# Performance work log

Measured on AMD Instinct MI355X. Metric: run time of the kernel, lower is better.

## Reference

```python
import jax, jax.numpy as jnp
import numpy as np
from jax import lax

B, CIN, HID, COUT = 64, 256, 256, 10
MULTI, KS = 3, 3
TH = TW = 7      # template (kernel) input spatial size
SH = SW = 31     # search input spatial size
EPS = 1e-5
DN = ('NCHW', 'OIHW', 'NCHW')


def _conv(x, w):
    return lax.conv_general_dilated(x, w, (1, 1), 'VALID', dimension_numbers=DN)


def _bn(x, p):
    # p: [4, C] packed (gamma, beta, running_mean, running_var); inference-mode BN
    g, b, m, v = p[0], p[1], p[2], p[3]
    inv = g / jnp.sqrt(v + EPS)
    return x * inv[:, None, None] + (b - m * inv)[:, None, None]


def _dwxcorr(x, k):
    # per-sample depthwise cross-correlation via groups = B*C trick
    b, c, h, w = x.shape
    kh, kw = k.shape[2], k.shape[3]
    y = lax.conv_general_dilated(
        x.reshape(1, b * c, h, w), k.reshape(b * c, 1, kh, kw),
        (1, 1), 'VALID', dimension_numbers=DN, feature_group_count=b * c)
    return y.reshape(b, c, y.shape[2], y.shape[3])


def _multixcorr(search, kernel):
    # crop template feature to 5x5 / 3x3 / 1x1 sub-kernels, xcorr each,
    # center-crop outputs to the common (smallest) size, concat on channels
    kh = kernel.shape[2]
    feats = []
    for i in range(MULTI):
        kk = kernel[:, :, i:kh - i, i:kh - i]
        o = _dwxcorr(search, kk)
        if i > 0:
            o = o[:, :, i:o.shape[2] - i, i:o.shape[3] - i]
        feats.append(o)
    return jnp.concatenate(feats, axis=1)  # [B, MULTI*HID, 25, 25]


def setup_inputs() -> dict:
    key = jax.random.key(0)
    ks = jax.random.split(key, 12)
    f32 = jnp.float32
    return {
        'kernel': jax.random.normal(ks[0], (B, CIN, TH, TW), f32),
        'search': jax.random.normal(ks[1], (B, CIN, SH, SW), f32),
        'wk': jax.random.normal(ks[2], (HID, CIN, KS, KS), f32) * 0.05,
        'bnk': jax.random.uniform(ks[3], (4, HID), f32, 0.1, 1.0),
        'ws': jax.random.normal(ks[4], (HID, CIN, KS, KS), f32) * 0.05,
        'bns': jax.random.uniform(ks[5], (4, HID), f32, 0.1, 1.0),
        'wd': jax.random.normal(ks[6], (HID, CIN * MULTI, 1, 1), f32) * 0.05,
        'bnd': jax.random.uniform(ks[7], (4, HID), f32, 0.1, 1.0),
        'wh1': jax.random.normal(ks[8], (HID, HID, 1, 1), f32) * 0.05,
        'bnh': jax.random.uniform(ks[9], (4, HID), f32, 0.1, 1.0),
        'wh2': jax.random.normal(ks[10], (COUT, HID, 1, 1), f32) * 0.05,
        'bh2': jax.random.normal(ks[11], (COUT,), f32) * 0.05,
    }


def reference(kernel, search, wk, bnk, ws, bns, wd, bnd, wh1, bnh, wh2, bh2):
    k = jax.nn.relu(_bn(_conv(kernel, wk), bnk))   # [B, HID, 5, 5]
    s = jax.nn.relu(_bn(_conv(search, ws), bns))   # [B, HID, 29, 29]
    feature = _multixcorr(s, k)                    # [B, 3*HID, 25, 25]
    feature = _bn(_conv(feature, wd), bnd)         # [B, HID, 25, 25]
    h = jax.nn.relu(_bn(_conv(feature, wh1), bnh))
    out = _conv(h, wh2) + bh2[:, None, None]       # [B, COUT, 25, 25]
    return out
```

## Files before the change

kernel.cpp:

```cpp
#include <hip/hip_runtime.h>
#include <hip/hip_bf16.h>
#include <cstdint>
#include <cstddef>

#define EPSBN 1e-5f

typedef unsigned short u16;
typedef unsigned int u32;
typedef _Float16 f16;
typedef _Float16 f16x8 __attribute__((ext_vector_type(8)));
typedef float f32x4 __attribute__((ext_vector_type(4)));

__device__ __forceinline__ void async_copy16(void* lds, const void* g) {
    __builtin_amdgcn_global_load_lds(
        (const __attribute__((address_space(1))) u32*)g,
        (__attribute__((address_space(3))) u32*)lds, 16, 0, 0);
}

__global__ __launch_bounds__(256) void prep_all(
    const float* __restrict__ sin, f16* __restrict__ sa,
    const float* __restrict__ kin, f16* __restrict__ ka,
    const float* __restrict__ wk, const float* __restrict__ ws,
    const float* __restrict__ wd, const float* __restrict__ wh1,
    const float* __restrict__ wh2, f16* __restrict__ bpk,
    f16* __restrict__ bps, f16* __restrict__ bpd, f16* __restrict__ bp1,
    f16* __restrict__ bp2) {
    __shared__ float tile[64][65];
    int t = blockIdx.x;
    int tid = threadIdx.x;
    if (t < 4352) {
        int b = t / 68;
        int rem = t - b * 68;
        int c0 = (rem / 17) * 64;
        int z = rem % 17;
        bool isk = (z == 16);
        const float* in = isk ? kin : sin;
        f16* op = isk ? ka : sa;
        int HW = isk ? 49 : 961;
        int h0 = isk ? 0 : z * 64;
        int cl = tid >> 6;
        int hl = tid & 63;
        for (int r = cl; r < 64; r += 4) {
            int hw = h0 + hl;
            tile[r][hl] =
                (hw < HW) ? in[(size_t)(b * 256 + c0 + r) * HW + hw] : 0.f;
        }
        __syncthreads();
        int c = tid & 63;
        for (int r = cl; r < 64; r += 4) {
            int hw = h0 + r;
            if (hw < HW)
                op[((size_t)b * HW + hw) * 256 + c0 + c] = (f16)tile[c][r];
        }
        return;
    }
    int blk = t - 4352;
    const float* W;
    f16* Bp;
    int nK32, OCr, K, i;
    bool conv = false;
    if (blk < 2304) {
        W = wk; Bp = bpk; nK32 = 72; OCr = 256; K = 2304; conv = true;
        i = blk * 256 + tid;
    } else if (blk < 4608) {
        W = ws; Bp = bps; nK32 = 72; OCr = 256; K = 2304; conv = true;
        i = (blk - 2304) * 256 + tid;
    } else if (blk < 5376) {
        W = wd; Bp = bpd; nK32 = 24; OCr = 256; K = 768;
        i = (blk - 4608) * 256 + tid;
    } else if (blk < 5632) {
        W = wh1; Bp = bp1; nK32 = 8; OCr = 256; K = 256;
        i = (blk - 5376) * 256 + tid;
    } else {
        W = wh2; Bp = bp2; nK32 = 8; OCr = 10; K = 256;
        i = (blk - 5632) * 256 + tid;
    }
    int per = nK32 * 512;
    int oct = i / per;
    int r = i - oct * per;
    int k32 = r >> 9;
    int lr = r & 511;
    int l = lr >> 3, j = lr & 7;
    int oc = oct * 16 + (l & 15);
    int k = k32 * 32 + ((l >> 4) << 3) + j;
    float v = 0.f;
    if (oc < OCr)
        v = conv ? W[(size_t)(oc * 256 + (k & 255)) * 9 + (k >> 8)]
                 : W[(size_t)oc * K + k];
    Bp[(size_t)(oct * nK32 + k32) * 512 + lr] = (f16)v;
}

template <int KHW, int EPI>
__device__ __forceinline__ void gemm8_body(
    f16* lds, const f16* __restrict__ A, const f16* __restrict__ Bp,
    const float* __restrict__ bnp, float* __restrict__ outF,
    f16* __restrict__ oF, int m0, int M, int OC, int C, int H, int W,
    int OH, int OW) {
    const int Ktot = KHW * C;
    const int nKt = Ktot >> 6;
    const int nI = nKt >> 1;
    const int nK32 = Ktot >> 5;
    const int tid = threadIdx.x;
    const int lane = tid & 63;
    const int wid = tid >> 6;
    const int rowl = lane & 15;
    const int quad = lane >> 4;
    const int wm = wid >> 2;
    const int wn = wid & 3;
    const int OHW = OH * OW;

    int arow[4];
#pragma unroll
    for (int h = 0; h < 2; ++h)
#pragma unroll
        for (int s = 0; s < 2; ++s) {
            int ml = ((wid & 4) << 5) + h * 64 + (wid & 3) * 16 + s * 8 +
                     (lane >> 3);
            int m = m0 + ml;
            if (m >= M) m = M - 1;
            int b = m / OHW;
            int r = m - b * OHW;
            int y = r / OW;
            int x = r - y * OW;
            arow[h * 2 + s] = ((b * H + y) * W + x) * C +
                              (((lane & 7) ^ (lane >> 3)) << 3);
        }
    int bsrcb[2];
#pragma unroll
    for (int h = 0; h < 2; ++h) {
        int slot = h * 8 + wid;
        int o = ((slot >> 1) & 3) * 4 + ((slot >> 3) << 1) + (slot & 1);
        bsrcb[h] = o * nK32 * 512 + lane * 8;
    }

    auto koff_of = [&](int kt) {
        if (KHW == 9) {
            int pos = kt >> 2;
            int ky = pos / 3, kx = pos - ky * 3;
            return (ky * W + kx) * C + ((kt & 3) << 6);
        }
        return kt << 6;
    };
    auto stageA = [&](int buf, int h, int kt) {
        int koff = koff_of(kt);
#pragma unroll
        for (int s = 0; s < 2; ++s)
            async_copy16(
                &lds[buf * 16384 +
                     ((h * 1024 + wid * 128 + s * 64 + lane) << 3)],
                A + arow[h * 2 + s] + koff);
    };
    auto stageB = [&](int buf, int h, int kt) {
#pragma unroll
        for (int s = 0; s < 2; ++s)
            async_copy16(
                &lds[32768 + buf * 16384 +
                     ((((h * 8 + wid) * 2 + s) * 64 + lane) << 3)],
                Bp + bsrcb[h] + (kt * 2 + s) * 512);
    };

    f32x4 acc[8][4];
#pragma unroll
    for (int i = 0; i < 8; ++i)
#pragma unroll
        for (int j = 0; j < 4; ++j) acc[i][j] = (f32x4)0.f;

    f16x8 ah[4][2], bhA[2][2], bhB[2][2];

    auto dsA = [&](int buf, int qm) {
#pragma unroll
        for (int ii = 0; ii < 4; ++ii) {
            int g = qm * 128 + wm * 64 + ii * 16 + rowl;
#pragma unroll
            for (int ks = 0; ks < 2; ++ks)
                ah[ii][ks] = *(const f16x8*)&lds[
                    buf * 16384 + g * 64 +
                    ((((ks << 2) | quad) ^ (rowl & 7)) << 3)];
        }
    };
    auto dsB = [&](int buf, int qn, f16x8 (&bh)[2][2]) {
#pragma unroll
        for (int jj = 0; jj < 2; ++jj) {
            int slot = qn * 8 + wn * 2 + jj;
#pragma unroll
            for (int ks = 0; ks < 2; ++ks)
                bh[jj][ks] = *(const f16x8*)&lds[
                    32768 + buf * 16384 + (slot * 2 + ks) * 512 + lane * 8];
        }
    };

#define MFMA_QUAD(qm, qn, bh)                                            \
    do {                                                                 \
        _Pragma("unroll") for (int ks = 0; ks < 2; ++ks)                 \
            _Pragma("unroll") for (int ii = 0; ii < 4; ++ii)             \
                _Pragma("unroll") for (int jj = 0; jj < 2; ++jj)         \
                    acc[(qm)*4 + ii][(qn)*2 + jj] =                      \
                        __builtin_amdgcn_mfma_f32_16x16x32_f16(          \
                            ah[ii][ks], bh[jj][ks],                      \
                            acc[(qm)*4 + ii][(qn)*2 + jj], 0, 0, 0);     \
    } while (0)

#define PH_TAIL(MF)                                        \
    __builtin_amdgcn_s_barrier();                          \
    asm volatile("s_waitcnt lgkmcnt(0)" ::: "memory");     \
    __builtin_amdgcn_s_setprio(1);                         \
    MF;                                                    \
    __builtin_amdgcn_s_setprio(0)

    stageA(0, 0, 0);
    stageA(0, 1, 0);
    stageB(0, 0, 0);
    stageB(0, 1, 0);
    stageA(1, 0, 1);
    stageB(1, 0, 1);
    stageB(1, 1, 1);
    asm volatile("s_waitcnt vmcnt(6)" ::: "memory");
    __builtin_amdgcn_s_barrier();

    for (int it = 0; it < nI; ++it) {
        const bool more = (it + 1 < nI);
        const int t2 = 2 * it + 2;
        const int t3 = 2 * it + 3;
        dsA(0, 0);
        dsB(0, 0, bhA);
        stageA(1, 1, 2 * it + 1);
        PH_TAIL(MFMA_QUAD(0, 0, bhA));
        __builtin_amdgcn_s_barrier();
        dsB(0, 1, bhB);
        if (more) stageA(0, 0, t2);
        PH_TAIL(MFMA_QUAD(0, 1, bhB));
        __builtin_amdgcn_s_barrier();
        dsA(0, 1);
        if (more) stageB(0, 0, t2);
        PH_TAIL(MFMA_QUAD(1, 0, bhA));
        __builtin_amdgcn_s_barrier();
        if (more) stageB(0, 1, t2);
        PH_TAIL(MFMA_QUAD(1, 1, bhB));
        if (more)
            asm volatile("s_waitcnt vmcnt(6)" ::: "memory");
        else
            asm volatile("s_waitcnt vmcnt(0)" ::: "memory");
        __builtin_amdgcn_s_barrier();
        dsA(1, 0);
        dsB(1, 0, bhA);
        if (more) stageA(0, 1, t2);
        PH_TAIL(MFMA_QUAD(0, 0, bhA));
        __builtin_amdgcn_s_barrier();
        dsB(1, 1, bhB);
        if (more) stageA(1, 0, t3);
        PH_TAIL(MFMA_QUAD(0, 1, bhB));
        __builtin_amdgcn_s_barrier();
        dsA(1, 1);
        if (more) stageB(1, 0, t3);
        PH_TAIL(MFMA_QUAD(1, 0, bhA));
        __builtin_amdgcn_s_barrier();
        if (more) stageB(1, 1, t3);
        PH_TAIL(MFMA_QUAD(1, 1, bhB));
        if (more) asm volatile("s_waitcnt vmcnt(6)" ::: "memory");
        __builtin_amdgcn_s_barrier();
    }
#undef PH_TAIL
#undef MFMA_QUAD

#pragma unroll
    for (int j = 0; j < 4; ++j) {
        int oc = wn * 64 + j * 16 + rowl;
        bool ocv = oc < OC;
        float scale = 1.f, shift = 0.f;
        if (ocv) {
            if (EPI != 3) {
                float g = bnp[oc];
                float bb = bnp[OC + oc];
                float mm = bnp[2 * OC + oc];
                float vv = bnp[3 * OC + oc];
                float inv = g * rsqrtf(vv + EPSBN);
                scale = inv;
                shift = bb - mm * inv;
            } else {
                shift = bnp[oc];
            }
        }
#pragma unroll
        for (int i = 0; i < 8; ++i) {
#pragma unroll
            for (int r = 0; r < 4; ++r) {
                int m = m0 + wm * 128 + i * 16 + quad * 4 + r;
                if (m < M && ocv) {
                    float v = acc[i][j][r] * scale + shift;
                    if (EPI == 2) v = fmaxf(v, 0.f);
                    if (EPI == 3) {
                        int b = m / OHW;
                        int rr = m - b * OHW;
                        outF[((size_t)b * OC + oc) * OHW + rr] = v;
                    } else {
                        oF[(size_t)m * OC + oc] = (f16)v;
                    }
                }
            }
        }
    }
}

__global__ __launch_bounds__(512, 2) void conv33_fused8(
    const f16* sA_g, const f16* bpS, const float* bns, f16* sOut,
    const f16* kA_g, const f16* bpK, const float* bnk, f16* kOut) {
    __shared__ f16 lds[65536];
    bool sec = blockIdx.x < 7;
    const f16* A = sec ? kA_g : sA_g;
    const f16* Bp = sec ? bpK : bpS;
    const float* bnp = sec ? bnk : bns;
    f16* oF = sec ? kOut : sOut;
    int M = sec ? 1600 : 53824;
    int Hh = sec ? 7 : 31;
    int OHs = sec ? 5 : 29;
    int m0 = (sec ? blockIdx.x : (blockIdx.x - 7)) * 256;
    gemm8_body<9, 2>(lds, A, Bp, bnp, nullptr, oF, m0, M, 256, 256, Hh, Hh,
                     OHs, OHs);
}

template <int KHW, int EPI>
__device__ __forceinline__ void gemm_body(
    f16* sA, const f16* __restrict__ A, const f16* __restrict__ Bp,
    const float* __restrict__ bnp, float* __restrict__ outF,
    f16* __restrict__ oF, int m0, int n0, int M, int OC, int C, int H, int W,
    int OH, int OW) {
    const int Ktot = KHW * C;
    const int nKb = Ktot >> 7;
    const int nK32 = Ktot >> 5;
    const int tid = threadIdx.x;
    const int OHW = OH * OW;

    int abase[8];
#pragma unroll
    for (int s = 0; s < 8; ++s) {
        int idx = tid + s * 256;
        int ml = idx >> 4;
        int qs = (idx & 15) ^ (ml & 15);
        int m = m0 + ml;
        if (m >= M) m = M - 1;
        int b = m / OHW;
        int r = m - b * OHW;
        int y = r / OW;
        int x = r - y * OW;
        abase[s] = ((b * H + y) * W + x) * C + qs * 8;
    }

    f32x4 acc[4][4];
#pragma unroll
    for (int i = 0; i < 4; ++i)
#pragma unroll
        for (int j = 0; j < 4; ++j) acc[i][j] = (f32x4)0.f;

    const int lane = tid & 63;
    const int row = lane & 15;
    const int quad = lane >> 4;
    const int wv = tid >> 6;
    const int wm = (wv & 1) * 64;
    const int wn = (wv >> 1) * 64;
    const int octb = (n0 + wn) >> 4;

    auto koff_of = [&](int kb) {
        if (KHW == 9) {
            int pos = kb >> 1;
            int cin0 = (kb & 1) << 7;
            int ky = pos / 3;
            int kx = pos - ky * 3;
            return (ky * W + kx) * C + cin0;
        }
        return kb << 7;
    };
    auto issueA = [&](int bufbase, int kb) {
        int koff = koff_of(kb);
#pragma unroll
        for (int s = 0; s < 8; ++s)
            async_copy16(&sA[bufbase + tid * 8 + s * 2048],
                         A + abase[s] + koff);
    };
    auto loadB = [&](f16x8(&bh)[4][4], int kb) {
#pragma unroll
        for (int ks = 0; ks < 4; ++ks)
#pragma unroll
            for (int j = 0; j < 4; ++j)
                bh[ks][j] =
                    *(const f16x8*)&Bp[((size_t)(octb + j) * nK32 + kb * 4 +
                                        ks) *
                                           512 +
                                       lane * 8];
    };
    auto compute = [&](int bufbase, f16x8(&bh)[4][4]) {
#pragma unroll
        for (int ks = 0; ks < 4; ++ks) {
            f16x8 ah[4];
#pragma unroll
            for (int i = 0; i < 4; ++i) {
                int g = wm + i * 16 + row;
                ah[i] = *(const f16x8*)&sA[bufbase + g * 128 +
                                           ((((ks << 2) | quad) ^ row) << 3)];
            }
#pragma unroll
            for (int i = 0; i < 4; ++i)
#pragma unroll
                for (int j = 0; j < 4; ++j)
                    acc[i][j] = __builtin_amdgcn_mfma_f32_16x16x32_f16(
                        ah[i], bh[ks][j], acc[i][j], 0, 0, 0);
        }
    };

    f16x8 bh0[4][4], bh1[4][4];
    issueA(0, 0);
    loadB(bh0, 0);
    for (int kb = 0; kb < nKb; kb += 2) {
        __syncthreads();
        issueA(16384, kb + 1);
        loadB(bh1, kb + 1);
        compute(0, bh0);
        __syncthreads();
        if (kb + 2 < nKb) {
            issueA(0, kb + 2);
            loadB(bh0, kb + 2);
        }
        compute(16384, bh1);
    }

#pragma unroll
    for (int j = 0; j < 4; ++j) {
        int oc = n0 + wn + j * 16 + row;
        bool ocv = oc < OC;
        float scale = 1.f, shift = 0.f;
        if (ocv) {
            if (EPI != 3) {
                float g = bnp[oc];
                float bb = bnp[OC + oc];
                float mm = bnp[2 * OC + oc];
                float vv = bnp[3 * OC + oc];
                float inv = g * rsqrtf(vv + EPSBN);
                scale = inv;
                shift = bb - mm * inv;
            } else {
                shift = bnp[oc];
            }
        }
#pragma unroll
        for (int i = 0; i < 4; ++i) {
#pragma unroll
            for (int r = 0; r < 4; ++r) {
                int m = m0 + wm + i * 16 + quad * 4 + r;
                if (m < M && ocv) {
                    float v = acc[i][j][r] * scale + shift;
                    if (EPI == 2) v = fmaxf(v, 0.f);
                    if (EPI == 3) {
                        int b = m / OHW;
                        int rr = m - b * OHW;
                        outF[((size_t)b * OC + oc) * OHW + rr] = v;
                    } else {
                        oF[(size_t)m * OC + oc] = (f16)v;
                    }
                }
            }
        }
    }
}

template <int EPI>
__global__ __launch_bounds__(256, 2) void gemm_1x1(
    const f16* __restrict__ A, const f16* __restrict__ Bp,
    const float* __restrict__ bnp, float* __restrict__ outF,
    f16* __restrict__ oF, int M, int OC, int C) {
    __shared__ f16 sA[32768];
    gemm_body<1, EPI>(sA, A, Bp, bnp, outF, oF, blockIdx.x * 128,
                      blockIdx.y * 128, M, OC, C, 25, 25, 25, 25);
}

__global__ __launch_bounds__(256) void xcorr_nhwc(
    const f16* __restrict__ sf, const f16* __restrict__ kf,
    f16* __restrict__ feat) {
    int by = blockIdx.x;
    int b = by / 25;
    int y = by - b * 25;
    int c = threadIdx.x;
    float kv[25];
#pragma unroll
    for (int p = 0; p < 25; ++p)
        kv[p] = (float)kf[(size_t)(b * 25 + p) * 256 + c];
    const f16* srow = sf + (size_t)(b * 29 + y) * 29 * 256 + c;
    float sv[25];
#pragma unroll
    for (int d = 0; d < 5; ++d)
#pragma unroll
        for (int e = 0; e < 5; ++e)
            sv[d * 5 + e] = (float)srow[(size_t)(d * 29 + e) * 256];
    for (int x = 0;; ++x) {
        float a0 = 0.f, a1 = 0.f, a2;
#pragma unroll
        for (int p = 0; p < 25; ++p) a0 = fmaf(sv[p], kv[p], a0);
#pragma unroll
        for (int d = 1; d < 4; ++d)
#pragma unroll
            for (int e = 1; e < 4; ++e)
                a1 = fmaf(sv[d * 5 + e], kv[d * 5 + e], a1);
        a2 = sv[12] * kv[12];
        size_t o = ((size_t)by * 25 + x) * 768 + c;
        feat[o] = (f16)a0;
        feat[o + 256] = (f16)a1;
        feat[o + 512] = (f16)a2;
        if (x == 24) break;
#pragma unroll
        for (int d = 0; d < 5; ++d) {
#pragma unroll
            for (int e = 0; e < 4; ++e) sv[d * 5 + e] = sv[d * 5 + e + 1];
            sv[d * 5 + 4] = (float)srow[(size_t)(d * 29 + x + 5) * 256];
        }
    }
}

extern "C" void kernel_launch(void* const* d_in, const int* in_sizes, int n_in,
                              void* d_out, int out_size, void* d_ws,
                              size_t ws_size, hipStream_t stream) {
    const float* kernel_in = (const float*)d_in[0];
    const float* search_in = (const float*)d_in[1];
    const float* wk = (const float*)d_in[2];
    const float* bnk = (const float*)d_in[3];
    const float* ws = (const float*)d_in[4];
    const float* bns = (const float*)d_in[5];
    const float* wd = (const float*)d_in[6];
    const float* bnd = (const float*)d_in[7];
    const float* wh1 = (const float*)d_in[8];
    const float* bnh = (const float*)d_in[9];
    const float* wh2 = (const float*)d_in[10];
    const float* bh2 = (const float*)d_in[11];
    float* out = (float*)d_out;

    char* base = (char*)d_ws;
    size_t off = 0;
    auto alloc = [&](size_t bytes) {
        off = (off + 511) & ~(size_t)511;
        void* p = base + off;
        off += bytes;
        return p;
    };

    f16* bpd = (f16*)alloc((size_t)16 * 24 * 512 * 2);
    f16* bp1 = (f16*)alloc((size_t)16 * 8 * 512 * 2);
    f16* bp2 = (f16*)alloc((size_t)8 * 8 * 512 * 2);
    size_t Pf = (off + 511) & ~(size_t)511;
    f16* kfeat = (f16*)alloc((size_t)1600 * 256 * 2);
    f16* sfeat = (f16*)alloc((size_t)53824 * 256 * 2);
    size_t P1 = (off + 511) & ~(size_t)511;
    f16* bpk = (f16*)alloc((size_t)16 * 72 * 512 * 2);
    f16* bps = (f16*)alloc((size_t)16 * 72 * 512 * 2);
    f16* ka = (f16*)alloc((size_t)64 * 49 * 256 * 2);
    f16* sa = (f16*)alloc((size_t)64 * 961 * 256 * 2);
    f16* feat = (f16*)(base + P1);
    f16* f2 = (f16*)(base + Pf);
    f16* hb = (f16*)(base + P1);

    prep_all<<<dim3(10112), 256, 0, stream>>>(search_in, sa, kernel_in, ka,
                                              wk, ws, wd, wh1, wh2, bpk, bps,
                                              bpd, bp1, bp2);
    conv33_fused8<<<dim3(218), 512, 0, stream>>>(sa, bps, bns, sfeat, ka,
                                                 bpk, bnk, kfeat);
    xcorr_nhwc<<<dim3(1600), 256, 0, stream>>>(sfeat, kfeat, feat);
    gemm_1x1<1><<<dim3(313, 2), 256, 0, stream>>>(feat, bpd, bnd, nullptr, f2,
                                                  40000, 256, 768);
    gemm_1x1<2><<<dim3(313, 2), 256, 0, stream>>>(f2, bp1, bnh, nullptr, hb,
                                                  40000, 256, 256);
    gemm_1x1<3><<<dim3(313, 1), 256, 0, stream>>>(hb, bp2, bh2, out, nullptr,
                                                  40000, 10, 256);
}
```

Measured before the change: 312.1 us.

## Fuse the three 1x1 head GEMMs into one kernel keeping intermediates in LDS

Replaces three separate gemm_1x1 launches (downsample with BN, hidden conv with BN and ReLU, output conv with bias) with one head_fused kernel. Each block handles 80 rows across all 256 channels and writes the intermediate f16 tiles into swizzled LDS, so they never go to global memory. This removes two launches and the global write and read of the two 40000x256 intermediates. In exchange, each block now computes all output channels (500 blocks with 4 waves each), and the final 10-channel GEMM runs on only one wave per block.

```diff
diff --git a/kernel.cpp b/kernel.cpp
--- a/kernel.cpp
+++ b/kernel.cpp
@@ -318,157 +318,183 @@
                      OHs, OHs);
 }
 
-template <int KHW, int EPI>
-__device__ __forceinline__ void gemm_body(
-    f16* sA, const f16* __restrict__ A, const f16* __restrict__ Bp,
-    const float* __restrict__ bnp, float* __restrict__ outF,
-    f16* __restrict__ oF, int m0, int n0, int M, int OC, int C, int H, int W,
-    int OH, int OW) {
-    const int Ktot = KHW * C;
-    const int nKb = Ktot >> 7;
-    const int nK32 = Ktot >> 5;
+__global__ __launch_bounds__(256, 2) void head_fused(
+    const f16* __restrict__ feat, const f16* __restrict__ bpd,
+    const float* __restrict__ bnd, const f16* __restrict__ bp1,
+    const float* __restrict__ bnh, const f16* __restrict__ bp2,
+    const float* __restrict__ bh2, float* __restrict__ out) {
+    __shared__ f16 lds[40960];
+    const int F2B = 20480;
     const int tid = threadIdx.x;
-    const int OHW = OH * OW;
-
-    int abase[8];
-#pragma unroll
-    for (int s = 0; s < 8; ++s) {
+    const int lane = tid & 63;
+    const int rowl = lane & 15;
+    const int quad = lane >> 4;
+    const int wn = tid >> 6;
+    const int m0 = blockIdx.x * 80;
+
+    int asrc[5];
+#pragma unroll
+    for (int s = 0; s < 5; ++s) {
         int idx = tid + s * 256;
         int ml = idx >> 4;
         int qs = (idx & 15) ^ (ml & 15);
-        int m = m0 + ml;
-        if (m >= M) m = M - 1;
-        int b = m / OHW;
-        int r = m - b * OHW;
-        int y = r / OW;
-        int x = r - y * OW;
-        abase[s] = ((b * H + y) * W + x) * C + qs * 8;
-    }
-
-    f32x4 acc[4][4];
-#pragma unroll
-    for (int i = 0; i < 4; ++i)
+        asrc[s] = ml * 768 + qs * 8;
+    }
+    auto issueA = [&](int buf, int kb) {
+#pragma unroll
+        for (int s = 0; s < 5; ++s)
+            async_copy16(&lds[buf * 10240 + (tid + s * 256) * 8],
+                         feat + (size_t)m0 * 768 + asrc[s] + kb * 128);
+    };
+    auto loadB = [&](f16x8(&bh)[4][4], const f16* __restrict__ Bp, int nK32,
+                     int kb) {
+#pragma unroll
+        for (int ks = 0; ks < 4; ++ks)
+#pragma unroll
+            for (int j = 0; j < 4; ++j)
+                bh[ks][j] = *(const f16x8*)&Bp[((size_t)((wn * 4 + j) * nK32 +
+                                                         kb * 4 + ks)) *
+                                                   512 +
+                                               lane * 8];
+    };
+
+    f32x4 acc[5][4];
+#pragma unroll
+    for (int i = 0; i < 5; ++i)
 #pragma unroll
         for (int j = 0; j < 4; ++j) acc[i][j] = (f32x4)0.f;
 
-    const int lane = tid & 63;
-    const int row = lane & 15;
-    const int quad = lane >> 4;
-    const int wv = tid >> 6;
-    const int wm = (wv & 1) * 64;
-    const int wn = (wv >> 1) * 64;
-    const int octb = (n0 + wn) >> 4;
-
-    auto koff_of = [&](int kb) {
-        if (KHW == 9) {
-            int pos = kb >> 1;
-            int cin0 = (kb & 1) << 7;
-            int ky = pos / 3;
-            int kx = pos - ky * 3;
-            return (ky * W + kx) * C + cin0;
-        }
-        return kb << 7;
-    };
-    auto issueA = [&](int bufbase, int kb) {
-        int koff = koff_of(kb);
-#pragma unroll
-        for (int s = 0; s < 8; ++s)
-            async_copy16(&sA[bufbase + tid * 8 + s * 2048],
-                         A + abase[s] + koff);
-    };
-    auto loadB = [&](f16x8(&bh)[4][4], int kb) {
-#pragma unroll
-        for (int ks = 0; ks < 4; ++ks)
-#pragma unroll
-            for (int j = 0; j < 4; ++j)
-                bh[ks][j] =
-                    *(const f16x8*)&Bp[((size_t)(octb + j) * nK32 + kb * 4 +
-                                        ks) *
-                                           512 +
-                                       lane * 8];
-    };
-    auto compute = [&](int bufbase, f16x8(&bh)[4][4]) {
+    auto computeS1 = [&](int buf, f16x8(&bh)[4][4]) {
 #pragma unroll
         for (int ks = 0; ks < 4; ++ks) {
-            f16x8 ah[4];
-#pragma unroll
-            for (int i = 0; i < 4; ++i) {
-                int g = wm + i * 16 + row;
-                ah[i] = *(const f16x8*)&sA[bufbase + g * 128 +
-                                           ((((ks << 2) | quad) ^ row) << 3)];
-            }
-#pragma unroll
-            for (int i = 0; i < 4; ++i)
+            f16x8 ah[5];
+#pragma unroll
+            for (int i = 0; i < 5; ++i)
+                ah[i] = *(const f16x8*)&lds[buf * 10240 +
+                                            (i * 16 + rowl) * 128 +
+                                            ((((ks << 2) | quad) ^ rowl)
+                                             << 3)];
+#pragma unroll
+            for (int i = 0; i < 5; ++i)
 #pragma unroll
                 for (int j = 0; j < 4; ++j)
                     acc[i][j] = __builtin_amdgcn_mfma_f32_16x16x32_f16(
                         ah[i], bh[ks][j], acc[i][j], 0, 0, 0);
         }
     };
+    auto tileRd = [&](int kb, int ks, int i) {
+        int g = i * 16 + rowl;
+        int kc = kb * 16 + (ks << 2) + quad;
+        int sw = (kc & 24) | ((kc ^ rowl) & 7);
+        return *(const f16x8*)&lds[F2B + g * 256 + (sw << 3)];
+    };
 
     f16x8 bh0[4][4], bh1[4][4];
     issueA(0, 0);
-    loadB(bh0, 0);
-    for (int kb = 0; kb < nKb; kb += 2) {
+    loadB(bh0, bpd, 24, 0);
+    for (int kb = 0; kb < 6; kb += 2) {
         __syncthreads();
-        issueA(16384, kb + 1);
-        loadB(bh1, kb + 1);
-        compute(0, bh0);
+        issueA(1, kb + 1);
+        loadB(bh1, bpd, 24, kb + 1);
+        computeS1(0, bh0);
         __syncthreads();
-        if (kb + 2 < nKb) {
+        if (kb + 2 < 6) {
             issueA(0, kb + 2);
-            loadB(bh0, kb + 2);
-        }
-        compute(16384, bh1);
-    }
-
+            loadB(bh0, bpd, 24, kb + 2);
+        }
+        computeS1(1, bh1);
+    }
 #pragma unroll
     for (int j = 0; j < 4; ++j) {
-        int oc = n0 + wn + j * 16 + row;
-        bool ocv = oc < OC;
-        float scale = 1.f, shift = 0.f;
-        if (ocv) {
-            if (EPI != 3) {
-                float g = bnp[oc];
-                float bb = bnp[OC + oc];
-                float mm = bnp[2 * OC + oc];
-                float vv = bnp[3 * OC + oc];
-                float inv = g * rsqrtf(vv + EPSBN);
-                scale = inv;
-                shift = bb - mm * inv;
-            } else {
-                shift = bnp[oc];
+        int oc = wn * 64 + j * 16 + rowl;
+        float g = bnd[oc], bb = bnd[256 + oc], mm = bnd[512 + oc],
+              vv = bnd[768 + oc];
+        float inv = g * rsqrtf(vv + EPSBN);
+        float shift = bb - mm * inv;
+        int c = oc >> 3;
+#pragma unroll
+        for (int i = 0; i < 5; ++i)
+#pragma unroll
+            for (int r = 0; r < 4; ++r) {
+                int row = i * 16 + quad * 4 + r;
+                int sw = (c & 24) | ((c ^ row) & 7);
+                lds[F2B + row * 256 + (sw << 3) + (oc & 7)] =
+                    (f16)(acc[i][j][r] * inv + shift);
             }
-        }
-#pragma unroll
-        for (int i = 0; i < 4; ++i) {
+    }
+    loadB(bh0, bp1, 8, 0);
+    __syncthreads();
+
+#pragma unroll
+    for (int i = 0; i < 5; ++i)
+#pragma unroll
+        for (int j = 0; j < 4; ++j) acc[i][j] = (f32x4)0.f;
+    loadB(bh1, bp1, 8, 1);
+#pragma unroll
+    for (int kb = 0; kb < 2; ++kb) {
+#pragma unroll
+        for (int ks = 0; ks < 4; ++ks) {
+            f16x8 ah[5];
+#pragma unroll
+            for (int i = 0; i < 5; ++i) ah[i] = tileRd(kb, ks, i);
+#pragma unroll
+            for (int i = 0; i < 5; ++i)
+#pragma unroll
+                for (int j = 0; j < 4; ++j)
+                    acc[i][j] = __builtin_amdgcn_mfma_f32_16x16x32_f16(
+                        ah[i], kb ? bh1[ks][j] : bh0[ks][j], acc[i][j], 0, 0,
+                        0);
+        }
+    }
+    __syncthreads();
+#pragma unroll
+    for (int j = 0; j < 4; ++j) {
+        int oc = wn * 64 + j * 16 + rowl;
+        float g = bnh[oc], bb = bnh[256 + oc], mm = bnh[512 + oc],
+              vv = bnh[768 + oc];
+        float inv = g * rsqrtf(vv + EPSBN);
+        float shift = bb - mm * inv;
+        int c = oc >> 3;
+#pragma unroll
+        for (int i = 0; i < 5; ++i)
 #pragma unroll
             for (int r = 0; r < 4; ++r) {
-                int m = m0 + wm + i * 16 + quad * 4 + r;
-                if (m < M && ocv) {
-                    float v = acc[i][j][r] * scale + shift;
-                    if (EPI == 2) v = fmaxf(v, 0.f);
-                    if (EPI == 3) {
-                        int b = m / OHW;
-                        int rr = m - b * OHW;
-                        outF[((size_t)b * OC + oc) * OHW + rr] = v;
-                    } else {
-                        oF[(size_t)m * OC + oc] = (f16)v;
-                    }
-                }
+                int row = i * 16 + quad * 4 + r;
+                int sw = (c & 24) | ((c ^ row) & 7);
+                lds[F2B + row * 256 + (sw << 3) + (oc & 7)] =
+                    (f16)fmaxf(acc[i][j][r] * inv + shift, 0.f);
             }
-        }
-    }
-}
-
-template <int EPI>
-__global__ __launch_bounds__(256, 2) void gemm_1x1(
-    const f16* __restrict__ A, const f16* __restrict__ Bp,
-    const float* __restrict__ bnp, float* __restrict__ outF,
-    f16* __restrict__ oF, int M, int OC, int C) {
-    __shared__ f16 sA[32768];
-    gemm_body<1, EPI>(sA, A, Bp, bnp, outF, oF, blockIdx.x * 128,
-                      blockIdx.y * 128, M, OC, C, 25, 25, 25, 25);
+    }
+    __syncthreads();
+    if (wn != 0) return;
+
+    f32x4 a3[5];
+#pragma unroll
+    for (int i = 0; i < 5; ++i) a3[i] = (f32x4)0.f;
+#pragma unroll
+    for (int kb = 0; kb < 2; ++kb)
+#pragma unroll
+        for (int ks = 0; ks < 4; ++ks) {
+            f16x8 b3 =
+                *(const f16x8*)&bp2[(size_t)(kb * 4 + ks) * 512 + lane * 8];
+#pragma unroll
+            for (int i = 0; i < 5; ++i)
+                a3[i] = __builtin_amdgcn_mfma_f32_16x16x32_f16(
+                    tileRd(kb, ks, i), b3, a3[i], 0, 0, 0);
+        }
+    int oc = rowl;
+    if (oc < 10) {
+        float shift = bh2[oc];
+#pragma unroll
+        for (int i = 0; i < 5; ++i)
+#pragma unroll
+            for (int r = 0; r < 4; ++r) {
+                int m = m0 + i * 16 + quad * 4 + r;
+                int b = m / 625;
+                int rr = m - b * 625;
+                out[((size_t)b * 10 + oc) * 625 + rr] = a3[i][r] + shift;
+            }
+    }
 }
 
 __global__ __launch_bounds__(256) void xcorr_nhwc(
@@ -542,7 +568,6 @@
     f16* bpd = (f16*)alloc((size_t)16 * 24 * 512 * 2);
     f16* bp1 = (f16*)alloc((size_t)16 * 8 * 512 * 2);
     f16* bp2 = (f16*)alloc((size_t)8 * 8 * 512 * 2);
-    size_t Pf = (off + 511) & ~(size_t)511;
     f16* kfeat = (f16*)alloc((size_t)1600 * 256 * 2);
     f16* sfeat = (f16*)alloc((size_t)53824 * 256 * 2);
     size_t P1 = (off + 511) & ~(size_t)511;
@@ -551,8 +576,6 @@
     f16* ka = (f16*)alloc((size_t)64 * 49 * 256 * 2);
     f16* sa = (f16*)alloc((size_t)64 * 961 * 256 * 2);
     f16* feat = (f16*)(base + P1);
-    f16* f2 = (f16*)(base + Pf);
-    f16* hb = (f16*)(base + P1);
 
     prep_all<<<dim3(10112), 256, 0, stream>>>(search_in, sa, kernel_in, ka,
                                               wk, ws, wd, wh1, wh2, bpk, bps,
@@ -560,10 +583,6 @@
     conv33_fused8<<<dim3(218), 512, 0, stream>>>(sa, bps, bns, sfeat, ka,
                                                  bpk, bnk, kfeat);
     xcorr_nhwc<<<dim3(1600), 256, 0, stream>>>(sfeat, kfeat, feat);
-    gemm_1x1<1><<<dim3(313, 2), 256, 0, stream>>>(feat, bpd, bnd, nullptr, f2,
-                                                  40000, 256, 768);
-    gemm_1x1<2><<<dim3(313, 2), 256, 0, stream>>>(f2, bp1, bnh, nullptr, hb,
-                                                  40000, 256, 256);
-    gemm_1x1<3><<<dim3(313, 1), 256, 0, stream>>>(hb, bp2, bh2, out, nullptr,
-                                                  40000, 10, 256);
-}
+    head_fused<<<dim3(500), 256, 0, stream>>>(feat, bpd, bnd, bp1, bnh, bp2,
+                                              bh2, out);
+}
```

After: 273.3 us. 1.14x faster.
